# Kernel tuning notes

Hardware: AMD Instinct MI355X
Metric: run time of the kernel (lower is better)

## Reference

```python
import jax, jax.numpy as jnp
import numpy as np

IN_DIM = 32000   # source vocab
OUT_DIM = 32000  # target vocab
HID = 1024
MAXLEN = 32      # decode steps
B = 64
SRC_LEN = 256


def _lstm_bias(h):
    # Keras LSTM: unit_forget_bias=True -> forget-gate bias = 1, rest 0. Gate order i,f,g,o.
    return jnp.concatenate([jnp.zeros(h), jnp.ones(h), jnp.zeros(2 * h)])


def setup_inputs() -> dict:
    key = jax.random.key(0)
    ks = jax.random.split(key, 12)
    g = lambda k, shape, s=0.02: (jax.random.normal(k, shape, jnp.float32) * s)
    return {
        "source": jax.random.randint(ks[0], (B, SRC_LEN), 0, IN_DIM, jnp.int32),
        "enc_emb": g(ks[1], (IN_DIM, HID)),
        "enc_K": g(ks[2], (HID, 4 * HID)),
        "enc_R": g(ks[3], (HID, 4 * HID)),
        "enc_b": _lstm_bias(HID),
        "dec_emb": g(ks[4], (OUT_DIM, HID)),
        "dec_K": g(ks[5], (HID, 4 * HID)),
        "dec_R": g(ks[6], (HID, 4 * HID)),
        "dec_b": _lstm_bias(HID),
        "W_a": g(ks[7], (HID, HID)),
        "W_c": g(ks[8], (2 * HID, HID)),
        "b_c": jnp.zeros(HID, jnp.float32),
        "W_out": g(ks[9], (HID, OUT_DIM)),
        "b_out": jnp.zeros(OUT_DIM, jnp.float32),
    }


def _lstm_cell(x, h, c, K, R, b):
    z = x @ K + h @ R + b
    i, f, g, o = jnp.split(z, 4, axis=-1)
    c = jax.nn.sigmoid(f) * c + jax.nn.sigmoid(i) * jnp.tanh(g)
    h = jax.nn.sigmoid(o) * jnp.tanh(c)
    return h, c


def reference(source, enc_emb, enc_K, enc_R, enc_b,
              dec_emb, dec_K, dec_R, dec_b,
              W_a, W_c, b_c, W_out, b_out):
    bsz = source.shape[0]
    hid = enc_K.shape[0]

    # ----- Encoder (mask_zero=True: skip state update where source==0) -----
    xe = enc_emb[source]                      # [B,T,H]
    mask = source > 0                         # [B,T]

    def enc_step(carry, xm):
        h, c = carry
        x, m = xm                             # x [B,H], m [B]
        hn, cn = _lstm_cell(x, h, c, enc_K, enc_R, enc_b)
        m = m[:, None]
        return (jnp.where(m, hn, h), jnp.where(m, cn, c)), jnp.where(m, hn, h)

    h0 = jnp.zeros((bsz, hid), xe.dtype)
    (he, ce), hs_t = jax.lax.scan(enc_step, (h0, h0),
                                  (xe.transpose(1, 0, 2), mask.T))
    hs = hs_t.transpose(1, 0, 2)              # [B,T,H] encoder states

    # ----- Decoder loop (greedy argmax feedback) -----
    hsW = hs @ W_a                            # [B,T,H], precomputed attention keys
    amask = mask[:, None, :].astype(hs.dtype)  # [B,1,T]

    def dec_step(carry, _):
        y, h, c = carry                       # y [B] int32
        x = dec_emb[y]                        # [B,H]
        hn, cn = _lstm_cell(x, h, c, dec_K, dec_R, dec_b)
        ht = hn[:, None, :]                   # [B,1,H]
        # Luong attention with source mask (exp -> mask -> normalize, as in source)
        sc = jnp.einsum('bqh,bkh->bqk', ht, hsW)        # [B,1,T]
        sc = jnp.exp(sc - sc.max(-1, keepdims=True)) * amask
        a = sc / sc.sum(-1, keepdims=True)
        ctx = jnp.einsum('bqk,bkh->bqh', a, hs)          # [B,1,H]
        ah = jnp.tanh(jnp.concatenate([ctx, ht], -1) @ W_c + b_c)
        prob = jax.nn.softmax(ah @ W_out + b_out, axis=-1)[:, 0, :]  # [B,V]
        yn = jnp.argmax(prob, axis=-1).astype(jnp.int32)
        return (yn, hn, cn), prob

    y0 = jnp.ones((bsz,), jnp.int32)          # start token = 1 (tf.ones)
    _, outs = jax.lax.scan(dec_step, (y0, he, ce), None, length=MAXLEN)
    return outs.transpose(1, 0, 2)            # [B, MAXLEN, OUT_DIM]
```

## Files before the change

### kernel.cpp

```cpp
#include <hip/hip_runtime.h>
#include <hip/hip_bf16.h>

typedef __hip_bfloat16 bf16;
typedef short bf8v __attribute__((ext_vector_type(8)));
typedef float f32x4 __attribute__((ext_vector_type(4)));

#define DEVINL __device__ __forceinline__
#define MFMA16(a, b, c) __builtin_amdgcn_mfma_f32_16x16x32_bf16((a), (b), (c), 0, 0, 0)

DEVINL float us2f(unsigned short u) { unsigned v = ((unsigned)u) << 16; return __uint_as_float(v); }
DEVINL float b2f(bf16 x) { return __bfloat162float(x); }
DEVINL bf16 f2b(float x) { return __float2bfloat16(x); }
DEVINL float sigf(float x) { return 1.0f / (1.0f + expf(-x)); }
DEVINL unsigned short f2bu(float f) { bf16 h = __float2bfloat16(f); return *(unsigned short*)&h; }

DEVINL void gload16(const void* g, void* l) {
  __builtin_amdgcn_global_load_lds((const __attribute__((address_space(1))) void*)g,
                                   (__attribute__((address_space(3))) void*)l, 16, 0, 0);
}

DEVINL unsigned ald(const unsigned* p) {
  return __hip_atomic_load(p, __ATOMIC_RELAXED, __HIP_MEMORY_SCOPE_AGENT);
}
DEVINL void ast(unsigned* p, unsigned v) {
  __hip_atomic_store(p, v, __ATOMIC_RELAXED, __HIP_MEMORY_SCOPE_AGENT);
}
DEVINL float aldf(const float* p) { unsigned u = ald((const unsigned*)p); return __uint_as_float(u); }
DEVINL void astf(float* p, float v) { ast((unsigned*)p, __float_as_uint(v)); }

DEVINL void gridbar2(unsigned* bars, unsigned lgen) {
  __syncthreads();
  if (threadIdx.x == 0) {
    unsigned s = lgen & 1;
    unsigned g = blockIdx.x >> 5;
    unsigned* grp = bars + (g * 2 + s) * 16;
    unsigned* top = bars + (16 + s) * 16;
    unsigned* gen = bars + 288;
    unsigned t = __hip_atomic_fetch_add(grp, 1u, __ATOMIC_RELAXED, __HIP_MEMORY_SCOPE_AGENT);
    if (t == 31u) {
      ast(grp, 0u);
      unsigned tt = __hip_atomic_fetch_add(top, 1u, __ATOMIC_RELAXED, __HIP_MEMORY_SCOPE_AGENT);
      if (tt == 7u) {
        ast(top, 0u);
        asm volatile("s_waitcnt vmcnt(0)");
        ast(gen, lgen + 1u);
      }
    }
    while (ald(gen) <= lgen) __builtin_amdgcn_s_sleep(4);
  }
  __syncthreads();
}

DEVINL void bar64(unsigned* b, unsigned lgen, int lid) {
  __syncthreads();
  if (threadIdx.x == 0) {
    unsigned s = lgen & 1;
    unsigned* grp = b + (((unsigned)(lid >> 5) & 1u) * 2 + s) * 16;
    unsigned* top = b + (4 + s) * 16;
    unsigned* gen = b + 96;
    unsigned t = __hip_atomic_fetch_add(grp, 1u, __ATOMIC_RELAXED, __HIP_MEMORY_SCOPE_AGENT);
    if (t == 31u) {
      ast(grp, 0u);
      unsigned tt = __hip_atomic_fetch_add(top, 1u, __ATOMIC_RELAXED, __HIP_MEMORY_SCOPE_AGENT);
      if (tt == 1u) {
        ast(top, 0u);
        asm volatile("s_waitcnt vmcnt(0)");
        ast(gen, lgen + 1u);
      }
    }
    while (ald(gen) <= lgen) __builtin_amdgcn_s_sleep(2);
  }
  __syncthreads();
}

#define OKPT_H  ((size_t)0)
#define OKPT_L  ((size_t)8388608)
#define ORPT_H  ((size_t)16777216)
#define ORPT_L  ((size_t)25165824)
#define OXE_H   ((size_t)35651584)
#define OXE_L   ((size_t)69206016)
#define OHSF5   ((size_t)35651584)
#define XCH     ((size_t)136314880)
#define OHPK_E0 (XCH + 0)
#define OHPK_E1 (XCH + 262144)
#define OHPK_D0 (XCH + 524288)
#define OCBUF5  (XCH + 1048576)
#define OAHPK   (XCH + 1310720)
#define ORSUM5  (XCH + 1572864)
#define ORMAX5  (XCH + 1638400)
#define ORIDX5  (XCH + 1769472)
#define OPSUM5  (XCH + 1900544)
#define OBARS5  (XCH + 1901568)
#define OYBUF   (XCH + 1917952)
#define OXK_L5  ((size_t)138412032)
#define OWCT_H  ((size_t)0)
#define OWCT_L  ((size_t)4194304)
#define OPCTX5  ((size_t)8388608)
#define OQBUF   ORPT_H
#define OWAB    (ORPT_H + 262144)
#define OWOT5   ((size_t)138412032)
#define OKRTH5  ((size_t)203948032)
#define OKRTL5  ((size_t)220725248)

#define DELTA   1e-4f

#define D_LH   0
#define D_LL   32768
#define D_ZS   65536
#define D_KBH  83968
#define D_KBL  116736
#define D4_A   0
#define D4_W   16384
#define D4_E   49152
#define D_WA   0
#define D_ES   65536
#define D_ZS3  0
#define D_PSC2 0
#define D_RV   0
#define D_RR   2048
#define D_CCN  4096
#define D_CAND 4160
#define D_RS   4224
#define D_RC   4352
#define D_YL   149504
#define D_INV  149568
#define D_RT   149632

__global__ void ed_zero_v8(float4* p, int n) {
  int i = blockIdx.x * 256 + threadIdx.x;
  if (i < n) p[i] = make_float4(0.f, 0.f, 0.f, 0.f);
}

__global__ void ed_cvt_v8(const float* __restrict__ in, bf16* __restrict__ out, int n) {
  int i = (blockIdx.x * 256 + threadIdx.x) * 4;
  if (i + 3 < n) {
    float4 v = *(const float4*)(in + i);
    ushort4 o;
    o.x = f2bu(v.x); o.y = f2bu(v.y); o.z = f2bu(v.z); o.w = f2bu(v.w);
    *(ushort4*)(out + i) = o;
  }
}

__global__ void ed_transpose_v8(const float* __restrict__ in, bf16* __restrict__ out,
                                int R, int C, int ostride, int ooff, int perm) {
  __shared__ float tile[32][33];
  int c0 = blockIdx.x * 32, r0 = blockIdx.y * 32;
  int tx = threadIdx.x & 31, ty0 = threadIdx.x >> 5;
#pragma unroll
  for (int i = 0; i < 4; i++) {
    int ty = ty0 + i * 8;
    tile[ty][tx] = in[(size_t)(r0 + ty) * C + c0 + tx];
  }
  __syncthreads();
#pragma unroll
  for (int i = 0; i < 4; i++) {
    int ty = ty0 + i * 8;
    int c = c0 + ty;
    int oc = perm ? ((c & 1023) * 4 + (c >> 10)) : c;
    out[(size_t)oc * ostride + ooff + r0 + tx] = f2b(tile[tx][ty]);
  }
}

__global__ void ed_transpose_split_v8(const float* __restrict__ in, bf16* __restrict__ oh,
                                      bf16* __restrict__ ol, int R, int C, int ostride,
                                      int ooff, int perm) {
  __shared__ float tile[32][33];
  int c0 = blockIdx.x * 32, r0 = blockIdx.y * 32;
  int tx = threadIdx.x & 31, ty0 = threadIdx.x >> 5;
#pragma unroll
  for (int i = 0; i < 4; i++) {
    int ty = ty0 + i * 8;
    tile[ty][tx] = in[(size_t)(r0 + ty) * C + c0 + tx];
  }
  __syncthreads();
#pragma unroll
  for (int i = 0; i < 4; i++) {
    int ty = ty0 + i * 8;
    int c = c0 + ty;
    int oc = perm ? ((c & 1023) * 4 + (c >> 10)) : c;
    float v = tile[tx][ty];
    bf16 hh = f2b(v);
    size_t o = (size_t)oc * ostride + ooff + r0 + tx;
    oh[o] = hh;
    ol[o] = f2b(v - b2f(hh));
  }
}

__global__ void ed_gather_split_v8(const int* __restrict__ src, const float* __restrict__ emb,
                                   bf16* __restrict__ xh, bf16* __restrict__ xl) {
  int bid = blockIdx.x;
  int t = bid >> 6, b = bid & 63;
  int tok = src[b * 256 + t];
  const float* rowp = emb + (size_t)tok * 1024;
  int i = threadIdx.x * 4;
  float4 v = *(const float4*)(rowp + i);
  bf16 h0 = f2b(v.x), h1 = f2b(v.y), h2 = f2b(v.z), h3 = f2b(v.w);
  ushort4 oh, ol;
  oh.x = *(unsigned short*)&h0; oh.y = *(unsigned short*)&h1;
  oh.z = *(unsigned short*)&h2; oh.w = *(unsigned short*)&h3;
  ol.x = f2bu(v.x - b2f(h0)); ol.y = f2bu(v.y - b2f(h1));
  ol.z = f2bu(v.z - b2f(h2)); ol.w = f2bu(v.w - b2f(h3));
  *(ushort4*)(xh + (size_t)bid * 1024 + i) = oh;
  *(ushort4*)(xl + (size_t)bid * 1024 + i) = ol;
}

__global__ __launch_bounds__(256, 2) void ed_gemm3_v8(
    const bf16* __restrict__ Ah, const bf16* __restrict__ Al,
    const bf16* __restrict__ Bh, const bf16* __restrict__ Bl,
    bf16* __restrict__ Ch, bf16* __restrict__ Cl, int M, int N, int K) {
  __shared__ __align__(16) bf16 Ash[128 * 32];
  __shared__ __align__(16) bf16 Asl[128 * 32];
  __shared__ __align__(16) bf16 Bsh[128 * 32];
  __shared__ __align__(16) bf16 Bsl[128 * 32];
  int m0 = blockIdx.y * 128, n0 = blockIdx.x * 128;
  int tid = threadIdx.x, w = tid >> 6, l = tid & 63;
  int wm = w >> 1, wn = w & 1;
  int lr = l & 15, lq = l >> 4;
  f32x4 acc[4][4] = {};
  for (int k0 = 0; k0 < K; k0 += 32) {
    __syncthreads();
#pragma unroll
    for (int j = 0; j < 2; j++) {
      int o = (w * 2 + j) * 1024 + l * 16;
      int rrow = o >> 6, kk = (o & 63) >> 1;
      gload16(Ah + (size_t)(m0 + rrow) * K + k0 + kk, (char*)Ash + (w * 2 + j) * 1024);
      gload16(Al + (size_t)(m0 + rrow) * K + k0 + kk, (char*)Asl + (w * 2 + j) * 1024);
      gload16(Bh + (size_t)(n0 + rrow) * K + k0 + kk, (char*)Bsh + (w * 2 + j) * 1024);
      gload16(Bl + (size_t)(n0 + rrow) * K + k0 + kk, (char*)Bsl + (w * 2 + j) * 1024);
    }
// ... 6 lines not shown
      for (int ni = 0; ni < 4; ni++) {
        bf8v b_h = *(const bf8v*)(Bsh + (wn * 64 + ni * 16 + lr) * 32 + lq * 8);
        bf8v b_l = *(const bf8v*)(Bsl + (wn * 64 + ni * 16 + lr) * 32 + lq * 8);
        acc[mi][ni] = MFMA16(a_h, b_h, acc[mi][ni]);
        acc[mi][ni] = MFMA16(a_h, b_l, acc[mi][ni]);
        acc[mi][ni] = MFMA16(a_l, b_h, acc[mi][ni]);
      }
    }
  }
#pragma unroll
  for (int mi = 0; mi < 4; mi++)
#pragma unroll
    for (int ni = 0; ni < 4; ni++)
#pragma unroll
      for (int r = 0; r < 4; r++) {
        float v = acc[mi][ni][r];
        bf16 hh = f2b(v);
        size_t idx = (size_t)(m0 + wm * 64 + mi * 16 + lq * 4 + r) * N + n0 + wn * 64 + ni * 16 + lr;
        Ch[idx] = hh;
        Cl[idx] = f2b(v - b2f(hh));
      }
}

__global__ __launch_bounds__(1024, 4) void ed_enc_v8(
    const int* __restrict__ src, const bf16* __restrict__ Rh, const bf16* __restrict__ Rl,
    const bf16* __restrict__ Xh, const bf16* __restrict__ Xl, const float* __restrict__ enc_b,
    unsigned* hpk0, unsigned* hpk1, float* __restrict__ cbuf,
    float* __restrict__ hsf, unsigned* barsE) {
  extern __shared__ char sm[];
  bf16* lh = (bf16*)sm;
  bf16* ll = (bf16*)(sm + 32768);
  float* zs = (float*)(sm + 65536);
  float* xkf = (float*)(sm + 82944);
  int bid = blockIdx.x, tid = threadIdx.x;
  int bg = bid >> 6, cg = bid & 63, lid = bid & 63;
  unsigned* barL = barsE + bg * 128;
  int wv = tid >> 6, l = tid & 63, lr = l & 15, lq = l >> 4;
  int kq = wv >> 2, cs = wv & 3;
  int srow = tid >> 6, sj0 = (tid & 63) * 16;
  int grow = tid >> 4, gul = tid & 15;
  bf8v Rh_[8], Rl_[8];
  {
    const bf16* bh = Rh + (size_t)(cg * 64 + cs * 16 + lr) * 1024 + kq * 256 + lq * 8;
    const bf16* bl = Rl + (size_t)(cg * 64 + cs * 16 + lr) * 1024 + kq * 256 + lq * 8;
#pragma unroll
    for (int i = 0; i < 8; i++) {
      Rh_[i] = *(const bf8v*)(bh + i * 32);
      Rl_[i] = *(const bf8v*)(bl + i * 32);
    }
  }
  float bi[4];
  float c_ = 0.f;
  if (tid < 256) {
#pragma unroll
    for (int g = 0; g < 4; g++) {
      int colp = cg * 64 + gul * 4 + g;
      bi[g] = enc_b[(colp & 3) * 1024 + (colp >> 2)];
    }
// ... 51 lines not shown
                xkf[grow * 64 + cc] + bi[g];
      }
      float iv = sigf(zz[0]), fv = sigf(zz[1]), gv = tanhf(zz[2]), ov = sigf(zz[3]);
      float cn = fv * c_ + iv * gv;
      float hnv = ov * tanhf(cn);
      bool m = src[b_ * 256 + t] > 0;
      int es = u ^ ((grow & 7) << 3);
      float hold = b2f(*(const bf16*)((char*)lh + grow * 2048 + es * 2)) +
                   b2f(*(const bf16*)((char*)ll + grow * 2048 + es * 2));
      float hv = m ? hnv : hold;
      c_ = m ? cn : c_;
      unsigned short uh = f2bu(hv);
      unsigned pkv = ((unsigned)uh << 16) | (unsigned)f2bu(hv - us2f(uh));
      ast(hn + (size_t)b_ * 1024 + u, pkv);
      hsf[((size_t)t * 64 + b_) * 1024 + u] = hv;
    }
    bar64(barL, lgen, lid);
    lgen++;
    unsigned* tp = hc; hc = hn; hn = tp;
  }
  if (tid < 256) cbuf[(size_t)(bg * 16 + grow) * 1024 + cg * 16 + gul] = c_;
}

DEVINL void dec_lstm8(int bg, int cgl, int tid, char* sm,
                      const unsigned* hc, unsigned* hn,
                      const float* __restrict__ dec_emb,
                      const bf16* __restrict__ Kh, const bf16* __restrict__ Kl,
                      const float* __restrict__ dec_b, float& c_) {
  bf16* lh = (bf16*)(sm + D_LH);
  bf16* ll = (bf16*)(sm + D_LL);
  {
    int srow = tid >> 6, sl = tid & 63;
    const unsigned* hrow = hc + (size_t)(bg * 16 + srow) * 1024 + sl * 16;
    unsigned u[16];
#pragma unroll
    for (int j = 0; j < 16; j++) u[j] = ald(hrow + j);
    uint4 ha, hb, la, lb;
    ha.x = (u[0] >> 16) | (u[1] & 0xffff0000u);  ha.y = (u[2] >> 16) | (u[3] & 0xffff0000u);
    ha.z = (u[4] >> 16) | (u[5] & 0xffff0000u);  ha.w = (u[6] >> 16) | (u[7] & 0xffff0000u);
    hb.x = (u[8] >> 16) | (u[9] & 0xffff0000u);  hb.y = (u[10] >> 16) | (u[11] & 0xffff0000u);
    hb.z = (u[12] >> 16) | (u[13] & 0xffff0000u); hb.w = (u[14] >> 16) | (u[15] & 0xffff0000u);
    la.x = (u[0] & 0xffffu) | (u[1] << 16);  la.y = (u[2] & 0xffffu) | (u[3] << 16);
    la.z = (u[4] & 0xffffu) | (u[5] << 16);  la.w = (u[6] & 0xffffu) | (u[7] << 16);
    lb.x = (u[8] & 0xffffu) | (u[9] << 16);  lb.y = (u[10] & 0xffffu) | (u[11] << 16);
    lb.z = (u[12] & 0xffffu) | (u[13] << 16); lb.w = (u[14] & 0xffffu) | (u[15] << 16);
    int swz = (srow & 7) << 4;
    char* rbh = (char*)lh + srow * 2048;
    char* rbl = (char*)ll + srow * 2048;
    *(uint4*)(rbh + ((sl * 32) ^ swz)) = ha;
    *(uint4*)(rbh + ((sl * 32 + 16) ^ swz)) = hb;
    *(uint4*)(rbl + ((sl * 32) ^ swz)) = la;
    *(uint4*)(rbl + ((sl * 32 + 16) ^ swz)) = lb;
  }
  int wv = tid >> 6, l = tid & 63, lr = l & 15, lq = l >> 4;
  int kg2 = wv >> 2, cs = wv & 3;
  bf16* kbh = (bf16*)(sm + D_KBH);
  bf16* kbl = (bf16*)(sm + D_KBL);
  const int* y_l = (const int*)(sm + D_YL);
  float* zs = (float*)(sm + D_ZS);
  f32x4 acc = {0.f, 0.f, 0.f, 0.f};
  int colB = cs * 16 + lr;
  int bswz = (colB & 7) << 4;
  int aswz = (lr & 7) << 4;
  for (int c = 0; c < 8; c++) {
    __syncthreads();
#pragma unroll
    for (int r = 0; r < 2; r++) {
      int i = wv * 128 + r * 64 + l;
      int col = i >> 5, j = i & 31;
      size_t se = (size_t)(cgl * 64 + col) * 2048 + c * 256 + ((size_t)(j ^ (col & 7)) << 3);
      gload16(Kh + se, (char*)kbh + wv * 2048 + r * 1024);
      gload16(Kl + se, (char*)kbl + wv * 2048 + r * 1024);
    }
    __syncthreads();
#pragma unroll
    for (int s = 0; s < 2; s++) {
      int kl = kg2 * 64 + s * 32 + lq * 8;
      bf8v b_h = *(const bf8v*)((char*)kbh + colB * 512 + ((kl * 2) ^ bswz));
      bf8v b_l = *(const bf8v*)((char*)kbl + colB * 512 + ((kl * 2) ^ bswz));
      int gk = c * 256 + kl;
      bf8v a_h, a_l;
      if (gk < 1024) {
        const float* xr = dec_emb + (size_t)y_l[lr] * 1024 + gk;
        float4 v0 = *(const float4*)xr;
        float4 v1 = *(const float4*)(xr + 4);
        float vs[8] = {v0.x, v0.y, v0.z, v0.w, v1.x, v1.y, v1.z, v1.w};
#pragma unroll
        for (int e = 0; e < 8; e++) {
          unsigned short uh = f2bu(vs[e]);
          a_h[e] = (short)uh;
          a_l[e] = (short)f2bu(vs[e] - us2f(uh));
        }
      } else {
        int hk = gk - 1024;
        a_h = *(const bf8v*)((char*)lh + lr * 2048 + ((hk * 2) ^ aswz));
        a_l = *(const bf8v*)((char*)ll + lr * 2048 + ((hk * 2) ^ aswz));
      }
      acc = MFMA16(a_h, b_h, acc);
      acc = MFMA16(a_h, b_l, acc);
      acc = MFMA16(a_l, b_h, acc);
      acc = MFMA16(a_l, b_l, acc);
    }
  }
#pragma unroll
  for (int r = 0; r < 4; r++) zs[(kg2 * 16 + lq * 4 + r) * 68 + cs * 16 + lr] = acc[r];
  __syncthreads();
  if (tid < 256) {
    int grow = tid >> 4, gul = tid & 15;
    int b_ = bg * 16 + grow;
    float zz[4];
#pragma unroll
    for (int g = 0; g < 4; g++) {
      int cc = gul * 4 + g;
      int colp = cgl * 64 + cc;
      float v = zs[(0 + grow) * 68 + cc] + zs[(16 + grow) * 68 + cc] +
                zs[(32 + grow) * 68 + cc] + zs[(48 + grow) * 68 + cc];
      zz[g] = v + dec_b[(colp & 3) * 1024 + (colp >> 2)];
    }
    float iv = sigf(zz[0]), fv = sigf(zz[1]), gv = tanhf(zz[2]), ov = sigf(zz[3]);
    float cn = fv * c_ + iv * gv;
    c_ = cn;
    float hv = ov * tanhf(cn);
    unsigned short uh = f2bu(hv);
    unsigned pkv = ((unsigned)uh << 16) | (unsigned)f2bu(hv - us2f(uh));
    ast(hn + (size_t)b_ * 1024 + cgl * 16 + gul, pkv);
  }
}

__global__ __launch_bounds__(1024, 4) void ed_dec_v8(
    const int* __restrict__ src,
    const bf16* __restrict__ KRh, const bf16* __restrict__ KRl, const float* __restrict__ dec_b,
    const bf16* __restrict__ WcTh, const bf16* __restrict__ WcTl, const float* __restrict__ b_cp,
    const bf16* __restrict__ WoTh, const float* __restrict__ b_op,
    const float* __restrict__ Wout_f32, const float* __restrict__ dec_emb,
    const bf16* __restrict__ WaB, float* __restrict__ qbuf,
    const float* __restrict__ hsf,
    unsigned* hpkA, unsigned* hpkB, float* __restrict__ cbuf,
    float* __restrict__ pctx, float* __restrict__ psum, unsigned* ahpk,
    float* __restrict__ rowsum, float* __restrict__ rmax, int* __restrict__ ridx,
    unsigned* ybuf, float* __restrict__ out, unsigned* barsG, unsigned* barsL) {
  extern __shared__ char sm[];
  int bid = blockIdx.x, tid = threadIdx.x;
  int bg = bid >> 6, cgl = bid & 63, lid = bid & 63;
  unsigned* barL = barsL + bg * 128;
  int wv = tid >> 6, l = tid & 63, lr = l & 15, lq = l >> 4;
  float c_ = 0.f;
  if (tid < 256) c_ = cbuf[(size_t)(bg * 16 + (tid >> 4)) * 1024 + cgl * 16 + (tid & 15)];
  unsigned *hc = hpkA, *hn = hpkB;
  unsigned lgenL = 0, lgenG = 0;

  if (tid < 16) ((int*)(sm + D_YL))[tid] = 1;
  __syncthreads();
  dec_lstm8(bg, cgl, tid, sm, hc, hn, dec_emb, KRh, KRl, dec_b, c_);
  bar64(barL, lgenL, lid); lgenL++;
  { unsigned* tp = hc; hc = hn; hn = tp; }

  for (int st = 0; st < 32; st++) {
    if (cgl < 16) {
      int colb = cgl * 64;
      int kq = wv >> 2, nq = wv & 3;
      float* zs = (float*)(sm + D_ZS);
      f32x4 acc = {0.f, 0.f, 0.f, 0.f};
      const unsigned* hrow = hc + (size_t)(bg * 16 + lr) * 1024;
      const bf16* warow = WaB + (size_t)(colb + nq * 16 + lr) * 1024;
#pragma unroll
      for (int i = 0; i < 8; i++) {
        int k = kq * 256 + i * 32 + lq * 8;
        bf8v a;
        const unsigned* hp = hrow + k;
#pragma unroll
        for (int e = 0; e < 8; e++) a[e] = (short)(ald(hp + e) >> 16);
        bf8v b = *(const bf8v*)(warow + k);
        acc = MFMA16(a, b, acc);
      }
#pragma unroll
      for (int r = 0; r < 4; r++) zs[(kq * 16 + lq * 4 + r) * 68 + nq * 16 + lr] = acc[r];
      __syncthreads();
      {
        int mrow = tid >> 6, col = tid & 63;
        float v = zs[(0 + mrow) * 68 + col] + zs[(16 + mrow) * 68 + col] +
                  zs[(32 + mrow) * 68 + col] + zs[(48 + mrow) * 68 + col];
        astf(qbuf + (size_t)(bg * 16 + mrow) * 1024 + colb + col, v);
      }
    }
    bar64(barL, lgenL, lid); lgenL++;
    {
      int b_ = bid >> 2, kg = bid & 3;
      float* wacc = (float*)(sm + D_WA);
      float* es = (float*)(sm + D_ES);
      float qr[16];
      {
        const float* qb = qbuf + (size_t)b_ * 1024 + l * 16;
        *(float4*)&qr[0]  = *(const float4*)(qb);
        *(float4*)&qr[4]  = *(const float4*)(qb + 4);
        *(float4*)&qr[8]  = *(const float4*)(qb + 8);
        *(float4*)&qr[12] = *(const float4*)(qb + 12);
      }
      float a16[16];
#pragma unroll
      for (int j = 0; j < 16; j++) a16[j] = 0.f;
      float esum = 0.f;
#pragma unroll
      for (int i = 0; i < 4; i++) {
        int kglob = kg * 64 + wv * 4 + i;
        const float* hrow = hsf + ((size_t)kglob * 64 + b_) * 1024 + l * 16;
        float4 v0 = *(const float4*)hrow;
        float4 v1 = *(const float4*)(hrow + 4);
        float4 v2 = *(const float4*)(hrow + 8);
        float4 v3 = *(const float4*)(hrow + 12);
        float vv[16] = {v0.x, v0.y, v0.z, v0.w, v1.x, v1.y, v1.z, v1.w,
// ... 65 lines not shown
              a_h[e] = (short)(u >> 16);
              a_l[e] = (short)(u & 0xffffu);
            }
          }
          bf8v b_h = *(const bf8v*)(bh + k);
          bf8v b_l = *(const bf8v*)(bl + k);
          acc = MFMA16(a_h, b_h, acc); acc = MFMA16(a_h, b_l, acc);
          acc = MFMA16(a_l, b_h, acc); acc = MFMA16(a_l, b_l, acc);
        }
#pragma unroll
        for (int r = 0; r < 4; r++) zs3[(kq * 16 + lq * 4 + r) * 17 + lr] = acc[r];
      }
      __syncthreads();
      if (tid < 256) {
        int grow = tid >> 4, gcol = tid & 15;
        float v = 0.f;
#pragma unroll
        for (int q = 0; q < 16; q++) v += zs3[(q * 16 + grow) * 17 + gcol];
        v += b_cp[cgl * 16 + gcol];
        float ahv = tanhf(v);
        unsigned short uh = f2bu(ahv);
        unsigned pkv = ((unsigned)uh << 16) | (unsigned)f2bu(ahv - us2f(uh));
        ast(ahpk + (size_t)(bg * 16 + grow) * 1024 + cgl * 16 + gcol, pkv);
      }
    }
    gridbar2(barsG, lgenG); lgenG++;
    {
      int base = bid * 125;
      bf16* abuf = (bf16*)(sm + D4_A);
      bf16* wbuf = (bf16*)(sm + D4_W);
      int rg = wv >> 2, cpair = wv & 3;
      f32x4 acc0 = {0.f, 0.f, 0.f, 0.f}, acc1 = {0.f, 0.f, 0.f, 0.f};
      for (int kc = 0; kc < 8; kc++) {
        int k0 = kc * 128;
        __syncthreads();
        {
          int row = tid >> 4, l16 = tid & 15;
          const unsigned* ap = ahpk + (size_t)row * 1024 + k0 + l16 * 8;
          unsigned u0 = ald(ap), u1 = ald(ap + 1), u2 = ald(ap + 2), u3 = ald(ap + 3);
          unsigned u4 = ald(ap + 4), u5 = ald(ap + 5), u6 = ald(ap + 6), u7 = ald(ap + 7);
          uint4 hv;
          hv.x = (u0 >> 16) | (u1 & 0xffff0000u);
          hv.y = (u2 >> 16) | (u3 & 0xffff0000u);
          hv.z = (u4 >> 16) | (u5 & 0xffff0000u);
          hv.w = (u6 >> 16) | (u7 & 0xffff0000u);
          *(uint4*)((char*)abuf + row * 256 + ((l16 * 16) ^ ((row & 7) << 4))) = hv;
        }
#pragma unroll
        for (int r = 0; r < 2; r++) {
          int i = wv * 128 + r * 64 + l;
          int col = i >> 4, j = i & 15;
          int ccol = col < 125 ? col : 124;
          size_t se = (size_t)(base + ccol) * 1024 + k0 + ((size_t)(j ^ (col & 7)) << 3);
          gload16(WoTh + se, (char*)wbuf + wv * 2048 + r * 1024);
        }
        __syncthreads();
#pragma unroll
        for (int s = 0; s < 4; s++) {
          int kl = s * 32 + lq * 8;
          int ar = rg * 16 + lr;
          bf8v a = *(const bf8v*)((char*)abuf + ar * 256 + ((kl * 2) ^ ((ar & 7) << 4)));
          int c0 = cpair * 32 + lr, c1 = c0 + 16;
          bf8v b0 = *(const bf8v*)((char*)wbuf + c0 * 256 + ((kl * 2) ^ ((c0 & 7) << 4)));
          bf8v b1 = *(const bf8v*)((char*)wbuf + c1 * 256 + ((kl * 2) ^ ((c1 & 7) << 4)));
          acc0 = MFMA16(a, b0, acc0);
          acc1 = MFMA16(a, b1, acc1);
        }
      }
      __syncthreads();
      float* e = (float*)(sm + D4_E);
      {
        int cl0 = cpair * 32 + lr;
        if (cl0 < 125) {
#pragma unroll
          for (int r = 0; r < 4; r++)
            e[(rg * 16 + lq * 4 + r) * 129 + cl0] = acc0[r] + b_op[base + cl0];
        }
        int cl1 = cpair * 32 + 16 + lr;
        if (cl1 < 125) {
#pragma unroll
          for (int r = 0; r < 4; r++)
            e[(rg * 16 + lq * 4 + r) * 129 + cl1] = acc1[r] + b_op[base + cl1];
        }
      }
      __syncthreads();
      if (tid < 64) {
        float sm_ = 0.f, v1 = -1e30f, v2 = -1e30f;
        int i1 = 0, i2 = 0;
        for (int c2 = 0; c2 < 125; c2++) {
          float v = e[tid * 129 + c2];
          sm_ += expf(v);
          if (v > v1) { v2 = v1; i2 = i1; v1 = v; i1 = base + c2; }
          else if (v > v2) { v2 = v; i2 = base + c2; }
        }
        astf(rowsum + bid * 64 + tid, sm_);
        astf(rmax + (bid * 64 + tid) * 2 + 0, v1);
        ast((unsigned*)ridx + (bid * 64 + tid) * 2 + 0, (unsigned)i1);
        astf(rmax + (bid * 64 + tid) * 2 + 1, v2);
        ast((unsigned*)ridx + (bid * 64 + tid) * 2 + 1, (unsigned)i2);
      }
    }
    gridbar2(barsG, lgenG); lgenG++;
    {
      float* psc2 = (float*)(sm + D_PSC2);
      {
        int rr = tid & 63, pp = tid >> 6;
        float s_ = 0.f;
#pragma unroll 4
        for (int cu = pp * 16; cu < pp * 16 + 16; cu++) s_ += aldf(rowsum + cu * 64 + rr);
        psc2[rr * 17 + pp] = s_;
      }
      __syncthreads();
      float* rt = (float*)(sm + D_RT);
      if (tid < 64) {
        float s_ = 0.f;
#pragma unroll
        for (int p2 = 0; p2 < 16; p2++) s_ += psc2[tid * 17 + p2];
        rt[tid] = s_;
      }
      __syncthreads();
      float* e = (float*)(sm + D4_E);
      {
        int base = bid * 125;
        for (int i = tid; i < 8000; i += 1024) {
          int r_ = i / 125, c2 = i - r_ * 125;
          float pv = expf(e[r_ * 129 + c2]) / rt[r_];
          __builtin_nontemporal_store(pv, out + ((size_t)r_ * 32 + st) * 32000 + base + c2);
        }
      }
      if (st < 31) {
        int* y_l = (int*)(sm + D_YL);
        if (cgl < 16) {
          int rowg = bg * 16 + cgl;
          float* rv = (float*)(sm + D_RV);
          float* rr2 = (float*)(sm + D_RR);
          int* ccnt = (int*)(sm + D_CCN);
          int* cand = (int*)(sm + D_CAND);
          double* rs = (double*)(sm + D_RS);
          int* rc = (int*)(sm + D_RC);
          float myv = -1e30f;
          if (tid < 512) {
            myv = aldf(rmax + ((size_t)(tid >> 1) * 64 + rowg) * 2 + (tid & 1));
            rv[tid] = myv;
            rr2[tid] = myv;
          }
          if (tid == 0) ccnt[0] = 0;
          __syncthreads();
          for (int w2 = 256; w2 >= 1; w2 >>= 1) {
            if (tid < w2) rr2[tid] = fmaxf(rr2[tid], rr2[tid + w2]);
            __syncthreads();
// ... 12 lines not shown
            double s_ = 0.0;
            for (int k = l; k < 1024; k += 64) {
              unsigned u = ald(ahpk + (size_t)rowg * 1024 + k);
              float av = us2f((unsigned short)(u >> 16)) + us2f((unsigned short)(u & 0xffffu));
              s_ += (double)av * (double)Wout_f32[(size_t)k * 32000 + c];
            }
#pragma unroll
            for (int off = 32; off > 0; off >>= 1) s_ += __shfl_down(s_, off);
            if (l == 0) { rs[wv] = s_ + (double)b_op[c]; rc[wv] = c; }
          }
          __syncthreads();
          if (tid == 0) {
            double bv = -1e30; int bc = 0x7fffffff;
            for (int ci = 0; ci < cnt; ci++) {
              double s_ = rs[ci]; int c = rc[ci];
              if (s_ > bv || (s_ == bv && c < bc)) { bv = s_; bc = c; }
            }
            ast(ybuf + rowg, (unsigned)bc);
          }
        }
        bar64(barL, lgenL, lid); lgenL++;
        if (tid < 16) y_l[tid] = (int)ald(ybuf + bg * 16 + tid);
        __syncthreads();
        dec_lstm8(bg, cgl, tid, sm, hc, hn, dec_emb, KRh, KRl, dec_b, c_);
      }
    }
    bar64(barL, lgenL, lid); lgenL++;
    { unsigned* tp = hc; hc = hn; hn = tp; }
  }
}

extern "C" void kernel_launch(void* const* d_in, const int* in_sizes, int n_in,
                              void* d_out, int out_size, void* d_ws, size_t ws_size,
                              hipStream_t stream) {
  (void)in_sizes; (void)n_in; (void)out_size; (void)ws_size;
  const int*   src     = (const int*)  d_in[0];
  const float* enc_emb = (const float*)d_in[1];
  const float* enc_K   = (const float*)d_in[2];
  const float* enc_R   = (const float*)d_in[3];
  const float* enc_b   = (const float*)d_in[4];
  const float* dec_emb = (const float*)d_in[5];
  const float* dec_K   = (const float*)d_in[6];
  const float* dec_R   = (const float*)d_in[7];
  const float* dec_b   = (const float*)d_in[8];
  const float* W_a     = (const float*)d_in[9];
  const float* W_c     = (const float*)d_in[10];
  const float* b_c     = (const float*)d_in[11];
  const float* W_out   = (const float*)d_in[12];
  const float* b_out   = (const float*)d_in[13];
  char* ws = (char*)d_ws;

  hipFuncSetAttribute((const void*)ed_enc_v8, hipFuncAttributeMaxDynamicSharedMemorySize, 163840);
  hipFuncSetAttribute((const void*)ed_dec_v8, hipFuncAttributeMaxDynamicSharedMemorySize, 163840);

  bf16* KpTh = (bf16*)(ws + OKPT_H);
  bf16* KpTl = (bf16*)(ws + OKPT_L);
  bf16* RpTh = (bf16*)(ws + ORPT_H);
  bf16* RpTl = (bf16*)(ws + ORPT_L);
  bf16* xeh  = (bf16*)(ws + OXE_H);
  bf16* xel  = (bf16*)(ws + OXE_L);
  float* hsf = (float*)(ws + OHSF5);
  unsigned* hpkE0 = (unsigned*)(ws + OHPK_E0);
  unsigned* hpkE1 = (unsigned*)(ws + OHPK_E1);
  unsigned* hpkD0 = (unsigned*)(ws + OHPK_D0);
  float* cbuf = (float*)(ws + OCBUF5);
  unsigned* ahpk = (unsigned*)(ws + OAHPK);
  float* rsum = (float*)(ws + ORSUM5);
  float* rmaxp = (float*)(ws + ORMAX5);
  int*  ridxp = (int*)(ws + ORIDX5);
  float* psum = (float*)(ws + OPSUM5);
  unsigned* barsE = (unsigned*)(ws + OBARS5);
  unsigned* barsG = (unsigned*)(ws + OBARS5 + 4096);
  unsigned* barsL = (unsigned*)(ws + OBARS5 + 8192);
  unsigned* ybuf = (unsigned*)(ws + OYBUF);
  bf16* XkL  = (bf16*)(ws + OXK_L5);
  bf16* XkH  = (bf16*)d_out;
  bf16* WcTh = (bf16*)(ws + OWCT_H);
  bf16* WcTl = (bf16*)(ws + OWCT_L);
  float* pctx = (float*)(ws + OPCTX5);
  float* qbuf = (float*)(ws + OQBUF);
  bf16* WaB  = (bf16*)(ws + OWAB);
  bf16* WoTh = (bf16*)(ws + OWOT5);
  bf16* KRTh = (bf16*)(ws + OKRTH5);
  bf16* KRTl = (bf16*)(ws + OKRTL5);

  ed_zero_v8<<<512, 256, 0, stream>>>((float4*)(ws + XCH), 131072);
  ed_transpose_split_v8<<<dim3(128, 32), 256, 0, stream>>>(enc_K, KpTh, KpTl, 1024, 4096, 1024, 0, 1);
  ed_transpose_split_v8<<<dim3(128, 32), 256, 0, stream>>>(enc_R, RpTh, RpTl, 1024, 4096, 1024, 0, 1);
  ed_gather_split_v8<<<16384, 256, 0, stream>>>(src, enc_emb, xeh, xel);
  ed_gemm3_v8<<<dim3(32, 128), 256, 0, stream>>>(xeh, xel, KpTh, KpTl, XkH, XkL, 16384, 4096, 1024);
  ed_transpose_split_v8<<<dim3(32, 64), 256, 0, stream>>>(W_c, WcTh, WcTl, 2048, 1024, 2048, 0, 0);
  ed_enc_v8<<<256, 1024, 87040, stream>>>(src, RpTh, RpTl, XkH, XkL, enc_b,
                                          hpkE0, hpkE1, cbuf, hsf, barsE);
  ed_cvt_v8<<<1024, 256, 0, stream>>>(W_a, WaB, 1048576);
  ed_transpose_v8<<<dim3(1000, 32), 256, 0, stream>>>(W_out, WoTh, 1024, 32000, 1024, 0, 0);
  ed_transpose_split_v8<<<dim3(128, 32), 256, 0, stream>>>(dec_K, KRTh, KRTl, 1024, 4096, 2048, 0, 1);
  ed_transpose_split_v8<<<dim3(128, 32), 256, 0, stream>>>(dec_R, KRTh, KRTl, 1024, 4096, 2048, 1024, 1);
  ed_dec_v8<<<256, 1024, 150528, stream>>>(src, KRTh, KRTl, dec_b, WcTh, WcTl, b_c,
                                           WoTh, b_out, W_out, dec_emb, WaB, qbuf, hsf,
                                           hpkE0, hpkD0, cbuf, pctx, psum, ahpk,
                                           rsum, rmaxp, ridxp, ybuf, (float*)d_out,
                                           barsG, barsL);
}
```

Measured before the change: 12.43 ms.

## Double-buffer decoder LSTM and vocab GEMM loads, remap block IDs per XCD

Result: faster. 12.17 ms (-2.2%).

```diff
diff --git a/kernel.cpp b/kernel.cpp
--- a/kernel.cpp
+++ b/kernel.cpp
@@ -28,11 +28,13 @@
 DEVINL float aldf(const float* p) { unsigned u = ald((const unsigned*)p); return __uint_as_float(u); }
 DEVINL void astf(float* p, float v) { ast((unsigned*)p, __float_as_uint(v)); }
 
+DEVINL int remap_lid(int bid) { return ((bid & 7) >> 1) * 64 + (((bid >> 3) << 1) | (bid & 1)); }
+
 DEVINL void gridbar2(unsigned* bars, unsigned lgen) {
   __syncthreads();
   if (threadIdx.x == 0) {
     unsigned s = lgen & 1;
-    unsigned g = blockIdx.x >> 5;
+    unsigned g = blockIdx.x & 7;
     unsigned* grp = bars + (g * 2 + s) * 16;
     unsigned* top = bars + (16 + s) * 16;
     unsigned* gen = bars + 288;
@@ -46,7 +48,7 @@
         ast(gen, lgen + 1u);
       }
     }
-    while (ald(gen) <= lgen) __builtin_amdgcn_s_sleep(4);
+    while (ald(gen) <= lgen) __builtin_amdgcn_s_sleep(2);
   }
   __syncthreads();
 }
@@ -68,7 +70,7 @@
         ast(gen, lgen + 1u);
       }
     }
-    while (ald(gen) <= lgen) __builtin_amdgcn_s_sleep(2);
+    while (ald(gen) <= lgen) __builtin_amdgcn_s_sleep(1);
   }
   __syncthreads();
 }
@@ -92,6 +94,7 @@
 #define OPSUM5  (XCH + 1900544)
 #define OBARS5  (XCH + 1901568)
 #define OYBUF   (XCH + 1917952)
+#define OAHB    (XCH + 1933312)
 #define OXK_L5  ((size_t)138412032)
 #define OWCT_H  ((size_t)0)
 #define OWCT_L  ((size_t)4194304)
@@ -107,31 +110,30 @@
 #define D_LH   0
 #define D_LL   32768
 #define D_ZS   65536
-#define D_KBH  83968
-#define D_KBL  116736
+#define D_KB   83968
 #define D4_A   0
-#define D4_W   16384
-#define D4_E   49152
+#define D4_W   32768
+#define D4_E   98304
 #define D_WA   0
 #define D_ES   65536
 #define D_ZS3  0
 #define D_PSC2 0
-#define D_RV   0
-#define D_RR   2048
-#define D_CCN  4096
-#define D_CAND 4160
-#define D_RS   4224
-#define D_RC   4352
+#define D_RV   8192
+#define D_RR   10240
+#define D_CCN  12288
+#define D_CAND 12352
+#define D_RS   12480
+#define D_RC   12608
 #define D_YL   149504
 #define D_INV  149568
 #define D_RT   149632
 
-__global__ void ed_zero_v8(float4* p, int n) {
+__global__ void ed_zero_v9(float4* p, int n) {
   int i = blockIdx.x * 256 + threadIdx.x;
   if (i < n) p[i] = make_float4(0.f, 0.f, 0.f, 0.f);
 }
 
-__global__ void ed_cvt_v8(const float* __restrict__ in, bf16* __restrict__ out, int n) {
+__global__ void ed_cvt_v9(const float* __restrict__ in, bf16* __restrict__ out, int n) {
   int i = (blockIdx.x * 256 + threadIdx.x) * 4;
   if (i + 3 < n) {
     float4 v = *(const float4*)(in + i);
@@ -141,7 +143,7 @@
   }
 }
 
-__global__ void ed_transpose_v8(const float* __restrict__ in, bf16* __restrict__ out,
+__global__ void ed_transpose_v9(const float* __restrict__ in, bf16* __restrict__ out,
                                 int R, int C, int ostride, int ooff, int perm) {
   __shared__ float tile[32][33];
   int c0 = blockIdx.x * 32, r0 = blockIdx.y * 32;
@@ -161,7 +163,7 @@
   }
 }
 
-__global__ void ed_transpose_split_v8(const float* __restrict__ in, bf16* __restrict__ oh,
+__global__ void ed_transpose_split_v9(const float* __restrict__ in, bf16* __restrict__ oh,
                                       bf16* __restrict__ ol, int R, int C, int ostride,
                                       int ooff, int perm) {
   __shared__ float tile[32][33];
@@ -186,7 +188,7 @@
   }
 }
 
-__global__ void ed_gather_split_v8(const int* __restrict__ src, const float* __restrict__ emb,
+__global__ void ed_gather_split_v9(const int* __restrict__ src, const float* __restrict__ emb,
                                    bf16* __restrict__ xh, bf16* __restrict__ xl) {
   int bid = blockIdx.x;
   int t = bid >> 6, b = bid & 63;
@@ -204,7 +206,7 @@
   *(ushort4*)(xl + (size_t)bid * 1024 + i) = ol;
 }
 
-__global__ __launch_bounds__(256, 2) void ed_gemm3_v8(
+__global__ __launch_bounds__(256, 2) void ed_gemm3_v9(
     const bf16* __restrict__ Ah, const bf16* __restrict__ Al,
     const bf16* __restrict__ Bh, const bf16* __restrict__ Bl,
     bf16* __restrict__ Ch, bf16* __restrict__ Cl, int M, int N, int K) {
@@ -257,7 +259,7 @@
       }
 }
 
-__global__ __launch_bounds__(1024, 4) void ed_enc_v8(
+__global__ __launch_bounds__(1024, 4) void ed_enc_v9(
     const int* __restrict__ src, const bf16* __restrict__ Rh, const bf16* __restrict__ Rl,
     const bf16* __restrict__ Xh, const bf16* __restrict__ Xl, const float* __restrict__ enc_b,
     unsigned* hpk0, unsigned* hpk1, float* __restrict__ cbuf,
@@ -268,7 +270,8 @@
   float* zs = (float*)(sm + 65536);
   float* xkf = (float*)(sm + 82944);
   int bid = blockIdx.x, tid = threadIdx.x;
-  int bg = bid >> 6, cg = bid & 63, lid = bid & 63;
+  int lid_all = remap_lid(bid);
+  int bg = lid_all >> 6, cg = lid_all & 63, lid = lid_all & 63;
   unsigned* barL = barsE + bg * 128;
   int wv = tid >> 6, l = tid & 63, lr = l & 15, lq = l >> 4;
   int kq = wv >> 2, cs = wv & 3;
@@ -366,13 +369,17 @@
   if (tid < 256) cbuf[(size_t)(bg * 16 + grow) * 1024 + cg * 16 + gul] = c_;
 }
 
-DEVINL void dec_lstm8(int bg, int cgl, int tid, char* sm,
+DEVINL void dec_lstm9(int bg, int cgl, int tid, char* sm,
                       const unsigned* hc, unsigned* hn,
                       const float* __restrict__ dec_emb,
                       const bf16* __restrict__ Kh, const bf16* __restrict__ Kl,
                       const float* __restrict__ dec_b, float& c_) {
   bf16* lh = (bf16*)(sm + D_LH);
   bf16* ll = (bf16*)(sm + D_LL);
+  int wv = tid >> 6, l = tid & 63, lr = l & 15, lq = l >> 4;
+  int kg2 = wv >> 2, cs = wv & 3;
+  const int* y_l = (const int*)(sm + D_YL);
+  float* zs = (float*)(sm + D_ZS);
   {
     int srow = tid >> 6, sl = tid & 63;
     const unsigned* hrow = hc + (size_t)(bg * 16 + srow) * 1024 + sl * 16;
@@ -396,47 +403,54 @@
     *(uint4*)(rbl + ((sl * 32) ^ swz)) = la;
     *(uint4*)(rbl + ((sl * 32 + 16) ^ swz)) = lb;
   }
-  int wv = tid >> 6, l = tid & 63, lr = l & 15, lq = l >> 4;
-  int kg2 = wv >> 2, cs = wv & 3;
-  bf16* kbh = (bf16*)(sm + D_KBH);
-  bf16* kbl = (bf16*)(sm + D_KBL);
-  const int* y_l = (const int*)(sm + D_YL);
-  float* zs = (float*)(sm + D_ZS);
+  bf8v xah[8], xal[8];
+  {
+    const float* xr = dec_emb + (size_t)y_l[lr] * 1024 + kg2 * 32 + lq * 8;
+#pragma unroll
+    for (int c = 0; c < 8; c++) {
+      float4 v0 = *(const float4*)(xr + c * 128);
+      float4 v1 = *(const float4*)(xr + c * 128 + 4);
+      float vs[8] = {v0.x, v0.y, v0.z, v0.w, v1.x, v1.y, v1.z, v1.w};
+#pragma unroll
+      for (int e = 0; e < 8; e++) {
+        unsigned short uh = f2bu(vs[e]);
+        xah[c][e] = (short)uh;
+        xal[c][e] = (short)f2bu(vs[e] - us2f(uh));
+      }
+    }
+  }
+  auto issueKB = [&](int c) {
+    int i = wv * 64 + l;
+    int col = i >> 4, j = i & 15;
+    size_t se = (size_t)(cgl * 64 + col) * 2048 + c * 128 + ((size_t)(j ^ (col & 7)) << 3);
+    char* dst = (char*)sm + D_KB + (c & 1) * 32768 + wv * 1024;
+    gload16(Kh + se, dst);
+    gload16(Kl + se, dst + 16384);
+  };
+  issueKB(0);
+  issueKB(1);
+  __syncthreads();
   f32x4 acc = {0.f, 0.f, 0.f, 0.f};
   int colB = cs * 16 + lr;
   int bswz = (colB & 7) << 4;
   int aswz = (lr & 7) << 4;
-  for (int c = 0; c < 8; c++) {
-    __syncthreads();
-#pragma unroll
-    for (int r = 0; r < 2; r++) {
-      int i = wv * 128 + r * 64 + l;
-      int col = i >> 5, j = i & 31;
-      size_t se = (size_t)(cgl * 64 + col) * 2048 + c * 256 + ((size_t)(j ^ (col & 7)) << 3);
-      gload16(Kh + se, (char*)kbh + wv * 2048 + r * 1024);
-      gload16(Kl + se, (char*)kbl + wv * 2048 + r * 1024);
-    }
-    __syncthreads();
-#pragma unroll
-    for (int s = 0; s < 2; s++) {
-      int kl = kg2 * 64 + s * 32 + lq * 8;
-      bf8v b_h = *(const bf8v*)((char*)kbh + colB * 512 + ((kl * 2) ^ bswz));
-      bf8v b_l = *(const bf8v*)((char*)kbl + colB * 512 + ((kl * 2) ^ bswz));
-      int gk = c * 256 + kl;
+#pragma unroll
+  for (int c = 0; c < 16; c++) {
+    if (c < 15) asm volatile("s_waitcnt vmcnt(2)" ::: "memory");
+    else        asm volatile("s_waitcnt vmcnt(0)" ::: "memory");
+    __builtin_amdgcn_s_barrier();
+    __builtin_amdgcn_sched_barrier(0);
+    {
+      int kl = kg2 * 32 + lq * 8;
+      const char* kb = (const char*)sm + D_KB + (c & 1) * 32768;
+      bf8v b_h = *(const bf8v*)(kb + colB * 256 + ((kl * 2) ^ bswz));
+      bf8v b_l = *(const bf8v*)(kb + 16384 + colB * 256 + ((kl * 2) ^ bswz));
       bf8v a_h, a_l;
-      if (gk < 1024) {
-        const float* xr = dec_emb + (size_t)y_l[lr] * 1024 + gk;
-        float4 v0 = *(const float4*)xr;
-        float4 v1 = *(const float4*)(xr + 4);
-        float vs[8] = {v0.x, v0.y, v0.z, v0.w, v1.x, v1.y, v1.z, v1.w};
-#pragma unroll
-        for (int e = 0; e < 8; e++) {
-          unsigned short uh = f2bu(vs[e]);
-          a_h[e] = (short)uh;
-          a_l[e] = (short)f2bu(vs[e] - us2f(uh));
-        }
+      if (c < 8) {
+        a_h = xah[c];
+        a_l = xal[c];
       } else {
-        int hk = gk - 1024;
+        int hk = (c - 8) * 128 + kl;
         a_h = *(const bf8v*)((char*)lh + lr * 2048 + ((hk * 2) ^ aswz));
         a_l = *(const bf8v*)((char*)ll + lr * 2048 + ((hk * 2) ^ aswz));
       }
@@ -445,6 +459,10 @@
       acc = MFMA16(a_l, b_h, acc);
       acc = MFMA16(a_l, b_l, acc);
     }
+    __builtin_amdgcn_sched_barrier(0);
+    __builtin_amdgcn_s_barrier();
+    __builtin_amdgcn_sched_barrier(0);
+    if (c + 2 < 16) issueKB(c + 2);
   }
 #pragma unroll
   for (int r = 0; r < 4; r++) zs[(kg2 * 16 + lq * 4 + r) * 68 + cs * 16 + lr] = acc[r];
@@ -471,7 +489,7 @@
   }
 }
 
-__global__ __launch_bounds__(1024, 4) void ed_dec_v8(
+__global__ __launch_bounds__(1024, 4) void ed_dec_v9(
     const int* __restrict__ src,
     const bf16* __restrict__ KRh, const bf16* __restrict__ KRl, const float* __restrict__ dec_b,
     const bf16* __restrict__ WcTh, const bf16* __restrict__ WcTl, const float* __restrict__ b_cp,
@@ -480,12 +498,13 @@
     const bf16* __restrict__ WaB, float* __restrict__ qbuf,
     const float* __restrict__ hsf,
     unsigned* hpkA, unsigned* hpkB, float* __restrict__ cbuf,
-    float* __restrict__ pctx, float* __restrict__ psum, unsigned* ahpk,
+    float* __restrict__ pctx, float* __restrict__ psum, unsigned* ahpk, unsigned* ahb32,
     float* __restrict__ rowsum, float* __restrict__ rmax, int* __restrict__ ridx,
     unsigned* ybuf, float* __restrict__ out, unsigned* barsG, unsigned* barsL) {
   extern __shared__ char sm[];
   int bid = blockIdx.x, tid = threadIdx.x;
-  int bg = bid >> 6, cgl = bid & 63, lid = bid & 63;
+  int lid_all = remap_lid(bid);
+  int bg = lid_all >> 6, cgl = lid_all & 63, lid = lid_all & 63;
   unsigned* barL = barsL + bg * 128;
   int wv = tid >> 6, l = tid & 63, lr = l & 15, lq = l >> 4;
   float c_ = 0.f;
@@ -495,9 +514,28 @@
 
   if (tid < 16) ((int*)(sm + D_YL))[tid] = 1;
   __syncthreads();
-  dec_lstm8(bg, cgl, tid, sm, hc, hn, dec_emb, KRh, KRl, dec_b, c_);
+  dec_lstm9(bg, cgl, tid, sm, hc, hn, dec_emb, KRh, KRl, dec_b, c_);
   bar64(barL, lgenL, lid); lgenL++;
   { unsigned* tp = hc; hc = hn; hn = tp; }
+
+  int p4base = lid_all * 125;
+  auto issueW4 = [&](int c) {
+#pragma unroll
+    for (int r = 0; r < 2; r++) {
+      int i = wv * 128 + r * 64 + l;
+      int col = i >> 4, j = i & 15;
+      int ccol = col < 125 ? col : 124;
+      size_t se = (size_t)(p4base + ccol) * 1024 + c * 128 + ((size_t)(j ^ (col & 7)) << 3);
+      gload16(WoTh + se, (char*)sm + D4_W + (c & 1) * 32768 + wv * 2048 + r * 1024);
+    }
+  };
+  auto stageA4 = [&](int ca) {
+    int row = tid >> 4, l16 = tid & 15;
+    const unsigned* ap = ahb32 + (size_t)row * 512 + ca * 64 + l16 * 4;
+    uint4 hv;
+    hv.x = ald(ap); hv.y = ald(ap + 1); hv.z = ald(ap + 2); hv.w = ald(ap + 3);
+    *(uint4*)((char*)sm + D4_A + (ca & 1) * 16384 + row * 256 + ((l16 ^ (row & 7)) << 4)) = hv;
+  };
 
   for (int st = 0; st < 32; st++) {
     if (cgl < 16) {
@@ -529,7 +567,7 @@
     }
     bar64(barL, lgenL, lid); lgenL++;
     {
-      int b_ = bid >> 2, kg = bid & 3;
+      int b_ = lid_all >> 2, kg = lid_all & 3;
       float* wacc = (float*)(sm + D_WA);
       float* es = (float*)(sm + D_ES);
       float qr[16];
@@ -641,50 +679,48 @@
         unsigned short uh = f2bu(ahv);
         unsigned pkv = ((unsigned)uh << 16) | (unsigned)f2bu(ahv - us2f(uh));
         ast(ahpk + (size_t)(bg * 16 + grow) * 1024 + cgl * 16 + gcol, pkv);
-      }
-    }
+        float ahn = __shfl_down(ahv, 1);
+        if ((tid & 1) == 0) {
+          unsigned pk2 = (unsigned)f2bu(ahv) | ((unsigned)f2bu(ahn) << 16);
+          ast(ahb32 + (size_t)(bg * 16 + grow) * 512 + cgl * 8 + (gcol >> 1), pk2);
+        }
+      }
+    }
+    issueW4(0);
+    issueW4(1);
     gridbar2(barsG, lgenG); lgenG++;
     {
-      int base = bid * 125;
-      bf16* abuf = (bf16*)(sm + D4_A);
-      bf16* wbuf = (bf16*)(sm + D4_W);
+      stageA4(0);
+      __syncthreads();
       int rg = wv >> 2, cpair = wv & 3;
       f32x4 acc0 = {0.f, 0.f, 0.f, 0.f}, acc1 = {0.f, 0.f, 0.f, 0.f};
-      for (int kc = 0; kc < 8; kc++) {
-        int k0 = kc * 128;
-        __syncthreads();
+#pragma unroll
+      for (int c = 0; c < 8; c++) {
+        if (c < 7) asm volatile("s_waitcnt vmcnt(2)" ::: "memory");
+        else       asm volatile("s_waitcnt vmcnt(0)" ::: "memory");
+        __builtin_amdgcn_s_barrier();
+        __builtin_amdgcn_sched_barrier(0);
         {
-          int row = tid >> 4, l16 = tid & 15;
-          const unsigned* ap = ahpk + (size_t)row * 1024 + k0 + l16 * 8;
-          unsigned u0 = ald(ap), u1 = ald(ap + 1), u2 = ald(ap + 2), u3 = ald(ap + 3);
-          unsigned u4 = ald(ap + 4), u5 = ald(ap + 5), u6 = ald(ap + 6), u7 = ald(ap + 7);
-          uint4 hv;
-          hv.x = (u0 >> 16) | (u1 & 0xffff0000u);
-          hv.y = (u2 >> 16) | (u3 & 0xffff0000u);
-          hv.z = (u4 >> 16) | (u5 & 0xffff0000u);
-          hv.w = (u6 >> 16) | (u7 & 0xffff0000u);
-          *(uint4*)((char*)abuf + row * 256 + ((l16 * 16) ^ ((row & 7) << 4))) = hv;
+          const char* wb = (const char*)sm + D4_W + (c & 1) * 32768;
+          const char* ab = (const char*)sm + D4_A + (c & 1) * 16384;
+          int ar = rg * 16 + lr;
+          int c0 = cpair * 32 + lr, c1 = c0 + 16;
+#pragma unroll
+          for (int s = 0; s < 4; s++) {
+            int kl = s * 32 + lq * 8;
+            bf8v a = *(const bf8v*)(ab + ar * 256 + (((s * 4 + lq) ^ (ar & 7)) << 4));
+            bf8v b0 = *(const bf8v*)(wb + c0 * 256 + ((kl * 2) ^ ((c0 & 7) << 4)));
+            bf8v b1 = *(const bf8v*)(wb + c1 * 256 + ((kl * 2) ^ ((c1 & 7) << 4)));
+            acc0 = MFMA16(a, b0, acc0);
+            acc1 = MFMA16(a, b1, acc1);
+          }
         }
-#pragma unroll
-        for (int r = 0; r < 2; r++) {
-          int i = wv * 128 + r * 64 + l;
-          int col = i >> 4, j = i & 15;
-          int ccol = col < 125 ? col : 124;
-          size_t se = (size_t)(base + ccol) * 1024 + k0 + ((size_t)(j ^ (col & 7)) << 3);
-          gload16(WoTh + se, (char*)wbuf + wv * 2048 + r * 1024);
-        }
-        __syncthreads();
-#pragma unroll
-        for (int s = 0; s < 4; s++) {
-          int kl = s * 32 + lq * 8;
-          int ar = rg * 16 + lr;
-          bf8v a = *(const bf8v*)((char*)abuf + ar * 256 + ((kl * 2) ^ ((ar & 7) << 4)));
-          int c0 = cpair * 32 + lr, c1 = c0 + 16;
-          bf8v b0 = *(const bf8v*)((char*)wbuf + c0 * 256 + ((kl * 2) ^ ((c0 & 7) << 4)));
-          bf8v b1 = *(const bf8v*)((char*)wbuf + c1 * 256 + ((kl * 2) ^ ((c1 & 7) << 4)));
-          acc0 = MFMA16(a, b0, acc0);
-          acc1 = MFMA16(a, b1, acc1);
-        }
+        if (c < 7) stageA4(c + 1);
+        asm volatile("s_waitcnt lgkmcnt(0)" ::: "memory");
+        __builtin_amdgcn_sched_barrier(0);
+        __builtin_amdgcn_s_barrier();
+        __builtin_amdgcn_sched_barrier(0);
+        if (c + 2 < 8) issueW4(c + 2);
       }
       __syncthreads();
       float* e = (float*)(sm + D4_E);
@@ -693,13 +729,13 @@
         if (cl0 < 125) {
 #pragma unroll
           for (int r = 0; r < 4; r++)
-            e[(rg * 16 + lq * 4 + r) * 129 + cl0] = acc0[r] + b_op[base + cl0];
+            e[(rg * 16 + lq * 4 + r) * 129 + cl0] = acc0[r] + b_op[p4base + cl0];
         }
         int cl1 = cpair * 32 + 16 + lr;
         if (cl1 < 125) {
 #pragma unroll
           for (int r = 0; r < 4; r++)
-            e[(rg * 16 + lq * 4 + r) * 129 + cl1] = acc1[r] + b_op[base + cl1];
+            e[(rg * 16 + lq * 4 + r) * 129 + cl1] = acc1[r] + b_op[p4base + cl1];
         }
       }
       __syncthreads();
@@ -709,14 +745,14 @@
         for (int c2 = 0; c2 < 125; c2++) {
           float v = e[tid * 129 + c2];
           sm_ += expf(v);
-          if (v > v1) { v2 = v1; i2 = i1; v1 = v; i1 = base + c2; }
-          else if (v > v2) { v2 = v; i2 = base + c2; }
+          if (v > v1) { v2 = v1; i2 = i1; v1 = v; i1 = p4base + c2; }
+          else if (v > v2) { v2 = v; i2 = p4base + c2; }
         }
-        astf(rowsum + bid * 64 + tid, sm_);
-        astf(rmax + (bid * 64 + tid) * 2 + 0, v1);
-        ast((unsigned*)ridx + (bid * 64 + tid) * 2 + 0, (unsigned)i1);
-        astf(rmax + (bid * 64 + tid) * 2 + 1, v2);
-        ast((unsigned*)ridx + (bid * 64 + tid) * 2 + 1, (unsigned)i2);
+        astf(rowsum + lid_all * 64 + tid, sm_);
+        astf(rmax + (lid_all * 64 + tid) * 2 + 0, v1);
+        ast((unsigned*)ridx + (lid_all * 64 + tid) * 2 + 0, (unsigned)i1);
+        astf(rmax + (lid_all * 64 + tid) * 2 + 1, v2);
+        ast((unsigned*)ridx + (lid_all * 64 + tid) * 2 + 1, (unsigned)i2);
       }
     }
     gridbar2(barsG, lgenG); lgenG++;
@@ -740,11 +776,10 @@
       __syncthreads();
       float* e = (float*)(sm + D4_E);
       {
-        int base = bid * 125;
         for (int i = tid; i < 8000; i += 1024) {
           int r_ = i / 125, c2 = i - r_ * 125;
           float pv = expf(e[r_ * 129 + c2]) / rt[r_];
-          __builtin_nontemporal_store(pv, out + ((size_t)r_ * 32 + st) * 32000 + base + c2);
+          __builtin_nontemporal_store(pv, out + ((size_t)r_ * 32 + st) * 32000 + p4base + c2);
         }
       }
       if (st < 31) {
@@ -803,7 +838,7 @@
         bar64(barL, lgenL, lid); lgenL++;
         if (tid < 16) y_l[tid] = (int)ald(ybuf + bg * 16 + tid);
         __syncthreads();
-        dec_lstm8(bg, cgl, tid, sm, hc, hn, dec_emb, KRh, KRl, dec_b, c_);
+        dec_lstm9(bg, cgl, tid, sm, hc, hn, dec_emb, KRh, KRl, dec_b, c_);
       }
     }
     bar64(barL, lgenL, lid); lgenL++;
@@ -831,8 +866,8 @@
   const float* b_out   = (const float*)d_in[13];
   char* ws = (char*)d_ws;
 
-  hipFuncSetAttribute((const void*)ed_enc_v8, hipFuncAttributeMaxDynamicSharedMemorySize, 163840);
-  hipFuncSetAttribute((const void*)ed_dec_v8, hipFuncAttributeMaxDynamicSharedMemorySize, 163840);
+  hipFuncSetAttribute((const void*)ed_enc_v9, hipFuncAttributeMaxDynamicSharedMemorySize, 163840);
+  hipFuncSetAttribute((const void*)ed_dec_v9, hipFuncAttributeMaxDynamicSharedMemorySize, 163840);
 
   bf16* KpTh = (bf16*)(ws + OKPT_H);
   bf16* KpTl = (bf16*)(ws + OKPT_L);
@@ -846,6 +881,7 @@
   unsigned* hpkD0 = (unsigned*)(ws + OHPK_D0);
   float* cbuf = (float*)(ws + OCBUF5);
   unsigned* ahpk = (unsigned*)(ws + OAHPK);
+  unsigned* ahb32 = (unsigned*)(ws + OAHB);
   float* rsum = (float*)(ws + ORSUM5);
   float* rmaxp = (float*)(ws + ORMAX5);
   int*  ridxp = (int*)(ws + ORIDX5);
@@ -865,21 +901,21 @@
   bf16* KRTh = (bf16*)(ws + OKRTH5);
   bf16* KRTl = (bf16*)(ws + OKRTL5);
 
-  ed_zero_v8<<<512, 256, 0, stream>>>((float4*)(ws + XCH), 131072);
-  ed_transpose_split_v8<<<dim3(128, 32), 256, 0, stream>>>(enc_K, KpTh, KpTl, 1024, 4096, 1024, 0, 1);
-  ed_transpose_split_v8<<<dim3(128, 32), 256, 0, stream>>>(enc_R, RpTh, RpTl, 1024, 4096, 1024, 0, 1);
-  ed_gather_split_v8<<<16384, 256, 0, stream>>>(src, enc_emb, xeh, xel);
-  ed_gemm3_v8<<<dim3(32, 128), 256, 0, stream>>>(xeh, xel, KpTh, KpTl, XkH, XkL, 16384, 4096, 1024);
-  ed_transpose_split_v8<<<dim3(32, 64), 256, 0, stream>>>(W_c, WcTh, WcTl, 2048, 1024, 2048, 0, 0);
-  ed_enc_v8<<<256, 1024, 87040, stream>>>(src, RpTh, RpTl, XkH, XkL, enc_b,
+  ed_zero_v9<<<512, 256, 0, stream>>>((float4*)(ws + XCH), 131072);
+  ed_transpose_split_v9<<<dim3(128, 32), 256, 0, stream>>>(enc_K, KpTh, KpTl, 1024, 4096, 1024, 0, 1);
+  ed_transpose_split_v9<<<dim3(128, 32), 256, 0, stream>>>(enc_R, RpTh, RpTl, 1024, 4096, 1024, 0, 1);
+  ed_gather_split_v9<<<16384, 256, 0, stream>>>(src, enc_emb, xeh, xel);
+  ed_gemm3_v9<<<dim3(32, 128), 256, 0, stream>>>(xeh, xel, KpTh, KpTl, XkH, XkL, 16384, 4096, 1024);
+  ed_transpose_split_v9<<<dim3(32, 64), 256, 0, stream>>>(W_c, WcTh, WcTl, 2048, 1024, 2048, 0, 0);
+  ed_enc_v9<<<256, 1024, 87040, stream>>>(src, RpTh, RpTl, XkH, XkL, enc_b,
                                           hpkE0, hpkE1, cbuf, hsf, barsE);
-  ed_cvt_v8<<<1024, 256, 0, stream>>>(W_a, WaB, 1048576);
-  ed_transpose_v8<<<dim3(1000, 32), 256, 0, stream>>>(W_out, WoTh, 1024, 32000, 1024, 0, 0);
-  ed_transpose_split_v8<<<dim3(128, 32), 256, 0, stream>>>(dec_K, KRTh, KRTl, 1024, 4096, 2048, 0, 1);
-  ed_transpose_split_v8<<<dim3(128, 32), 256, 0, stream>>>(dec_R, KRTh, KRTl, 1024, 4096, 2048, 1024, 1);
-  ed_dec_v8<<<256, 1024, 150528, stream>>>(src, KRTh, KRTl, dec_b, WcTh, WcTl, b_c,
+  ed_cvt_v9<<<1024, 256, 0, stream>>>(W_a, WaB, 1048576);
+  ed_transpose_v9<<<dim3(1000, 32), 256, 0, stream>>>(W_out, WoTh, 1024, 32000, 1024, 0, 0);
+  ed_transpose_split_v9<<<dim3(128, 32), 256, 0, stream>>>(dec_K, KRTh, KRTl, 1024, 4096, 2048, 0, 1);
+  ed_transpose_split_v9<<<dim3(128, 32), 256, 0, stream>>>(dec_R, KRTh, KRTl, 1024, 4096, 2048, 1024, 1);
+  ed_dec_v9<<<256, 1024, 150528, stream>>>(src, KRTh, KRTl, dec_b, WcTh, WcTl, b_c,
                                            WoTh, b_out, W_out, dec_emb, WaB, qbuf, hsf,
-                                           hpkE0, hpkD0, cbuf, pctx, psum, ahpk,
+                                           hpkE0, hpkD0, cbuf, pctx, psum, ahpk, ahb32,
                                            rsum, rmaxp, ridxp, ybuf, (float*)d_out,
                                            barsG, barsL);
 }
```
